# Kernel optimization log

Measured on AMD Instinct MI355X. Metric: run time of the kernel, lower is better.

Reference implementation:

```python
import jax, jax.numpy as jnp
import numpy as np

N = 50000      # nodes
E = 800000     # edges (avg degree 16)
F_IN = 3       # dataset.num_node_features
H = 256        # hidden_channels
G = 64         # batch_size (num graphs)
OUT = 24       # lin_out output dim


def setup_inputs() -> dict:
    key = jax.random.key(0)
    ks = jax.random.split(key, 16)
    s = 0.05
    inp = {
        "x": jax.random.normal(ks[0], (N, F_IN), jnp.float32),
        "edge_index": jax.random.randint(ks[1], (2, E), 0, N, dtype=jnp.int32),
        "batch": jnp.sort(jax.random.randint(ks[2], (N,), 0, G, dtype=jnp.int32)),
        # layer 1 (F_IN -> H)
        "w_rel1": jax.random.normal(ks[3], (F_IN, H), jnp.float32) * s,
        "w_root1": jax.random.normal(ks[4], (F_IN, H), jnp.float32) * s,
        "b1": jnp.zeros((H,), jnp.float32),
        # layers 2..7 (H -> H), stacked
        "w_rel": jax.random.normal(ks[5], (6, H, H), jnp.float32) * s,
        "w_root": jax.random.normal(ks[6], (6, H, H), jnp.float32) * s,
        "b": jnp.zeros((6, H), jnp.float32),
        # output head
        "w_out": jax.random.normal(ks[7], (H, OUT), jnp.float32) * s,
        "b_out": jnp.zeros((OUT,), jnp.float32),
    }
    return inp


def reference(x, edge_index, batch, w_rel1, w_root1, b1, w_rel, w_root, b, w_out, b_out):
    src, dst = edge_index[0], edge_index[1]

    def conv(h, wr, wro, bb):
        # PyG GraphConv with add aggregation:
        # out_i = W_rel @ sum_{j -> i} h_j + b + W_root @ h_i
        agg = jax.ops.segment_sum(h[src], dst, num_segments=N)
        return agg @ wr + h @ wro + bb

    h = jax.nn.relu(conv(x, w_rel1, w_root1, b1))
    for i in range(6):
        h = jax.nn.relu(conv(h, w_rel[i], w_root[i], b[i]))

    # global_mean_pool over batch segment ids
    counts = jax.ops.segment_sum(jnp.ones((N,), h.dtype), batch, num_segments=G)
    pooled = jax.ops.segment_sum(h, batch, num_segments=G) / jnp.maximum(counts, 1.0)[:, None]

    # dropout is identity in eval mode
    return pooled @ w_out + b_out
```

## Files before the change

kernel.cpp:

```cpp
#include <hip/hip_runtime.h>

#define N_NODES 50000
#define MPAD 50048
#define N_EDGES 800000
#define H 256
#define K_CAT 512
#define G_BATCH 64
#define OUT_DIM 24

#define SCAN_BLK 256
#define NBLK ((N_NODES + SCAN_BLK - 1) / SCAN_BLK)

typedef __attribute__((ext_vector_type(8))) short short8;
typedef __attribute__((ext_vector_type(4))) float float4v;

__device__ __forceinline__ float bf2f(unsigned short u) {
    return __uint_as_float(((unsigned)u) << 16);
}
__device__ __forceinline__ unsigned short f2bf(float f) {
    unsigned x = __float_as_uint(f);
    unsigned r = (x + 0x7FFFu + ((x >> 16) & 1u)) >> 16;
    return (unsigned short)r;
}

__device__ __forceinline__ void async_copy16(void* lds, const void* g) {
    __builtin_amdgcn_global_load_lds(
        (const __attribute__((address_space(1))) unsigned int*)g,
        (__attribute__((address_space(3))) unsigned int*)lds, 16, 0, 0);
}



__global__ void histo_kernel(const int* __restrict__ dst, int* __restrict__ deg,
                             int* __restrict__ epos) {
    int e = blockIdx.x * blockDim.x + threadIdx.x;
    if (e < N_EDGES) epos[e] = atomicAdd(&deg[dst[e]], 1);
}

__global__ void scan_block(const int* __restrict__ deg, int* __restrict__ rowptr,
                           int* __restrict__ blockSums) {
    __shared__ int s[SCAN_BLK];
    int idx = blockIdx.x * SCAN_BLK + threadIdx.x;
    int v = (idx < N_NODES) ? deg[idx] : 0;
    s[threadIdx.x] = v;
    __syncthreads();
    for (int off = 1; off < SCAN_BLK; off <<= 1) {
        int t = (threadIdx.x >= off) ? s[threadIdx.x - off] : 0;
        __syncthreads();
        s[threadIdx.x] += t;
        __syncthreads();
    }
    if (idx < N_NODES) rowptr[idx] = s[threadIdx.x] - v;
    if (threadIdx.x == SCAN_BLK - 1) blockSums[blockIdx.x] = s[threadIdx.x];
}

__global__ void scan_finish(int* __restrict__ rowptr, const int* __restrict__ blockSums) {
    __shared__ int s[SCAN_BLK];
    int t = threadIdx.x;
    int v = (t < NBLK) ? blockSums[t] : 0;
    s[t] = v;
    __syncthreads();
    for (int off = 1; off < SCAN_BLK; off <<= 1) {
        int tv = (t >= off) ? s[t - off] : 0;
        __syncthreads();
        s[t] += tv;
        __syncthreads();
    }
    int prefix = (blockIdx.x > 0) ? s[blockIdx.x - 1] : 0;
    int idx = blockIdx.x * SCAN_BLK + t;
    if (idx < N_NODES) rowptr[idx] += prefix;
    if (blockIdx.x == 0 && t == 0) rowptr[N_NODES] = s[NBLK - 1];
}

__global__ void fill_csr(const int* __restrict__ src, const int* __restrict__ dst,
                         const int* __restrict__ rowptr, const int* __restrict__ epos,
                         int* __restrict__ csr_src) {
    int e = blockIdx.x * blockDim.x + threadIdx.x;
    if (e >= N_EDGES) return;
    csr_src[rowptr[dst[e]] + epos[e]] = src[e];
}


__global__ void prep_weights(const float* __restrict__ w_rel, const float* __restrict__ w_root,
                             unsigned short* __restrict__ WcatT) {
    int idx = blockIdx.x * blockDim.x + threadIdx.x;
    if (idx >= 6 * K_CAT * H) return;
    int n = idx & (H - 1);
    int k = (idx >> 8) & (K_CAT - 1);
    int l = idx >> 17;
    float v;
    if (k < H) {
        int f = (k & 0xC0) | ((k & 3) << 4) | ((k >> 2) & 15);
        v = w_rel[(size_t)l * H * H + f * H + n];
    } else {
        v = w_root[(size_t)l * H * H + (k - H) * H + n];
    }
    WcatT[(size_t)l * H * K_CAT + (size_t)n * K_CAT + k] = f2bf(v);
}


__global__ void agg3(const float* __restrict__ x, const int* __restrict__ rowptr,
                     const int* __restrict__ csr_src, float* __restrict__ agg) {
    int n = blockIdx.x * blockDim.x + threadIdx.x;
    if (n >= N_NODES) return;
    int beg = rowptr[n], end = rowptr[n + 1];
    float a0 = 0.f, a1 = 0.f, a2 = 0.f;
    for (int i = beg; i < end; ++i) {
        int s = csr_src[i];
        a0 += x[s * 3 + 0];
        a1 += x[s * 3 + 1];
        a2 += x[s * 3 + 2];
    }
    agg[n * 3 + 0] = a0;
    agg[n * 3 + 1] = a1;
    agg[n * 3 + 2] = a2;
}

__global__ void layer1_kernel(const float* __restrict__ x, const float* __restrict__ agg,
                              const float* __restrict__ wr, const float* __restrict__ wro,
                              const float* __restrict__ bias, unsigned short* __restrict__ cat,
                              unsigned char* __restrict__ h8, float* __restrict__ hscale) {
    __shared__ unsigned char tmp[H];
    int n = blockIdx.x;
    int f = threadIdx.x;
    float a0 = agg[n * 3 + 0], a1 = agg[n * 3 + 1], a2 = agg[n * 3 + 2];
    float x0 = x[n * 3 + 0], x1 = x[n * 3 + 1], x2 = x[n * 3 + 2];
    float v = bias[f];
    v += a0 * wr[0 * H + f] + a1 * wr[1 * H + f] + a2 * wr[2 * H + f];
    v += x0 * wro[0 * H + f] + x1 * wro[1 * H + f] + x2 * wro[2 * H + f];
    v = fmaxf(v, 0.f);
    cat[(size_t)n * K_CAT + H + f] = f2bf(v);
    float m = v;
#pragma unroll
    for (int off = 1; off < 64; off <<= 1) m = fmaxf(m, __shfl_xor(m, off, 64));
    float inv = m > 0.f ? 255.f / m : 0.f;
    tmp[(f & 0xC0) | ((f & 15) << 2) | ((f >> 4) & 3)] = (unsigned char)(v * inv + 0.5f);
    if ((f & 63) == 0) hscale[n * 4 + (f >> 6)] = m * (1.f / 255.f);
    __syncthreads();
    if (f < 64) *(unsigned*)(h8 + (size_t)n * H + f * 4) = *(const unsigned*)(tmp + f * 4);
}


__global__ __launch_bounds__(256) void aggH(unsigned short* __restrict__ cat,
                                            const unsigned char* __restrict__ h8,
                                            const float* __restrict__ hscale,
                                            const int* __restrict__ rowptr,
                                            const int* __restrict__ csr_src) {
    int gtid = blockIdx.x * blockDim.x + threadIdx.x;
    int node = gtid >> 6;
    if (node >= N_NODES) return;
    int lane = threadIdx.x & 63;
    int sub = lane >> 4;
    int fl = lane & 15;
    int g = fl >> 2;
    int beg = rowptr[node], end = rowptr[node + 1];

    if (beg >= end) {
        if (sub == 0) {
            uint4 z = make_uint4(0, 0, 0, 0);
            unsigned short* o = cat + (size_t)node * K_CAT + fl * 16;
            *(uint4*)o = z;
            *(uint4*)(o + 8) = z;
        }
        return;
    }

    float acc[16] = {};
    const unsigned char* base = h8 + fl * 16;
    int last = end - 1;

    int i0 = beg + sub;
    int i1 = beg + 4 + sub;
    int i2 = beg + 8 + sub;
    int i3 = beg + 12 + sub;
    int s0 = csr_src[i0 < end ? i0 : last];
    int s1 = csr_src[i1 < end ? i1 : last];
    int s2 = csr_src[i2 < end ? i2 : last];
    int s3 = csr_src[i3 < end ? i3 : last];
    float sc0 = (i0 < end) ? hscale[s0 * 4 + g] : 0.f;
    float sc1 = (i1 < end) ? hscale[s1 * 4 + g] : 0.f;
    uint4 q0 = *(const uint4*)(base + (size_t)s0 * H);
    uint4 q1 = *(const uint4*)(base + (size_t)s1 * H);

    for (int i = beg; i < end; i += 4) {
        int i4 = i + 16 + sub;
        int s4 = csr_src[i4 < end ? i4 : last];
        int ic = i + 8 + sub;
        float sc2 = (ic < end) ? hscale[s2 * 4 + g] : 0.f;
        uint4 q2 = *(const uint4*)(base + (size_t)s2 * H);

        float sc = sc0;
        acc[0]  = fmaf((float)(q0.x & 0xffu), sc, acc[0]);
        acc[1]  = fmaf((float)((q0.x >> 8) & 0xffu), sc, acc[1]);
        acc[2]  = fmaf((float)((q0.x >> 16) & 0xffu), sc, acc[2]);
        acc[3]  = fmaf((float)(q0.x >> 24), sc, acc[3]);
        acc[4]  = fmaf((float)(q0.y & 0xffu), sc, acc[4]);
        acc[5]  = fmaf((float)((q0.y >> 8) & 0xffu), sc, acc[5]);
        acc[6]  = fmaf((float)((q0.y >> 16) & 0xffu), sc, acc[6]);
        acc[7]  = fmaf((float)(q0.y >> 24), sc, acc[7]);
        acc[8]  = fmaf((float)(q0.z & 0xffu), sc, acc[8]);
        acc[9]  = fmaf((float)((q0.z >> 8) & 0xffu), sc, acc[9]);
        acc[10] = fmaf((float)((q0.z >> 16) & 0xffu), sc, acc[10]);
        acc[11] = fmaf((float)(q0.z >> 24), sc, acc[11]);
        acc[12] = fmaf((float)(q0.w & 0xffu), sc, acc[12]);
        acc[13] = fmaf((float)((q0.w >> 8) & 0xffu), sc, acc[13]);
        acc[14] = fmaf((float)((q0.w >> 16) & 0xffu), sc, acc[14]);
        acc[15] = fmaf((float)(q0.w >> 24), sc, acc[15]);

        q0 = q1; q1 = q2;
        sc0 = sc1; sc1 = sc2;
        s2 = s3; s3 = s4;
    }

#pragma unroll
    for (int j = 0; j < 16; j++) {
        acc[j] += __shfl_xor(acc[j], 16, 64);
        acc[j] += __shfl_xor(acc[j], 32, 64);
    }

    if (sub == 0) {
        unsigned short* o = cat + (size_t)node * K_CAT + fl * 16;
        uint4 p0, p1;
        p0.x = (unsigned)f2bf(acc[0])  | ((unsigned)f2bf(acc[1]) << 16);
        p0.y = (unsigned)f2bf(acc[2])  | ((unsigned)f2bf(acc[3]) << 16);
        p0.z = (unsigned)f2bf(acc[4])  | ((unsigned)f2bf(acc[5]) << 16);
        p0.w = (unsigned)f2bf(acc[6])  | ((unsigned)f2bf(acc[7]) << 16);
        p1.x = (unsigned)f2bf(acc[8])  | ((unsigned)f2bf(acc[9]) << 16);
        p1.y = (unsigned)f2bf(acc[10]) | ((unsigned)f2bf(acc[11]) << 16);
        p1.z = (unsigned)f2bf(acc[12]) | ((unsigned)f2bf(acc[13]) << 16);
        p1.w = (unsigned)f2bf(acc[14]) | ((unsigned)f2bf(acc[15]) << 16);
        *(uint4*)o = p0;
        *(uint4*)(o + 8) = p1;
    }
}


#define GBM 64
#define GBN 128
#define GBK 64

__global__ __launch_bounds__(256) void gemm_mfma(
    const unsigned short* __restrict__ cat, const unsigned short* __restrict__ WcatT,
    const float* __restrict__ bias, unsigned short* __restrict__ catOut,
    unsigned char* __restrict__ h8, float* __restrict__ hscale) {
    __shared__ unsigned short sA[GBM][GBK];
    __shared__ unsigned short sB[GBN][GBK];

    const int tid = threadIdx.x;
    const int wave = tid >> 6;
    const int lane = tid & 63;
    const int quad = lane >> 4;
    const int l16 = lane & 15;
    const int wm0 = (wave & 1) * 32;
    const int wn0 = (wave >> 1) * 64;
    const int m0 = blockIdx.x * GBM;
    const int n0 = blockIdx.y * GBN;

    const int rowoff = lane >> 3;
    const int schunk = ((lane & 7) ^ rowoff) * 8;
    const unsigned short* Asrc[2];
    const unsigned short* Bsrc[4];
#pragma unroll
    for (int j = 0; j < 2; j++) {
        int q = wave * 2 + j;
        Asrc[j] = cat + (size_t)(m0 + q * 8 + rowoff) * K_CAT + schunk;
    }
#pragma unroll
    for (int j = 0; j < 4; j++) {
        int q = wave * 4 + j;
        Bsrc[j] = WcatT + (size_t)(n0 + q * 8 + rowoff) * K_CAT + schunk;
    }

    const int sw = l16 & 7;
    const int ca0 = (quad ^ sw) * 8;
    const int ca1 = ((4 + quad) ^ sw) * 8;

    float4v acc[2][4] = {};

    for (int kk = 0; kk < K_CAT; kk += GBK) {
#pragma unroll
        for (int j = 0; j < 2; j++)
            async_copy16((char*)sA + (wave * 2 + j) * 1024, Asrc[j] + kk);
#pragma unroll
        for (int j = 0; j < 4; j++)
            async_copy16((char*)sB + (wave * 4 + j) * 1024, Bsrc[j] + kk);
        __syncthreads();

        short8 a[2][2], b[4][2];
#pragma unroll
        for (int i = 0; i < 2; i++) {
            const unsigned short* ra = &sA[wm0 + i * 16 + l16][0];
            a[i][0] = *(const short8*)(ra + ca0);
            a[i][1] = *(const short8*)(ra + ca1);
        }
#pragma unroll
        for (int i = 0; i < 4; i++) {
            const unsigned short* rb = &sB[wn0 + i * 16 + l16][0];
            b[i][0] = *(const short8*)(rb + ca0);
            b[i][1] = *(const short8*)(rb + ca1);
        }
#pragma unroll
        for (int sub = 0; sub < 2; sub++)
#pragma unroll
            for (int mi = 0; mi < 2; mi++)
#pragma unroll
                for (int ni = 0; ni < 4; ni++)
                    acc[mi][ni] = __builtin_amdgcn_mfma_f32_16x16x32_bf16(
                        a[mi][sub], b[ni][sub], acc[mi][ni], 0, 0, 0);
        __syncthreads();
    }

    const int hb = n0 + wn0 + l16 * 4;
    const int gsc = (n0 + wn0) >> 6;
    float bcol[4];
#pragma unroll
    for (int ni = 0; ni < 4; ni++) bcol[ni] = bias[n0 + wn0 + ni * 16 + l16];

#pragma unroll
    for (int mi = 0; mi < 2; mi++) {
        int rowb = m0 + wm0 + mi * 16 + quad * 4;
#pragma unroll
        for (int r = 0; r < 4; r++) {
            int row = rowb + r;
            float v0 = fmaxf(acc[mi][0][r] + bcol[0], 0.f);
            float v1 = fmaxf(acc[mi][1][r] + bcol[1], 0.f);
            float v2 = fmaxf(acc[mi][2][r] + bcol[2], 0.f);
            float v3 = fmaxf(acc[mi][3][r] + bcol[3], 0.f);
            unsigned short* co = catOut + (size_t)row * K_CAT + H + n0 + wn0 + l16;
            co[0]  = f2bf(v0);
            co[16] = f2bf(v1);
            co[32] = f2bf(v2);
            co[48] = f2bf(v3);
            float m = fmaxf(fmaxf(v0, v1), fmaxf(v2, v3));
            m = fmaxf(m, __shfl_xor(m, 1, 64));
            m = fmaxf(m, __shfl_xor(m, 2, 64));
            m = fmaxf(m, __shfl_xor(m, 4, 64));
            m = fmaxf(m, __shfl_xor(m, 8, 64));
            float inv = m > 0.f ? 255.f / m : 0.f;
            unsigned p = (unsigned)(v0 * inv + 0.5f)
                       | ((unsigned)(v1 * inv + 0.5f) << 8)
                       | ((unsigned)(v2 * inv + 0.5f) << 16)
                       | ((unsigned)(v3 * inv + 0.5f) << 24);
            *(unsigned*)(h8 + (size_t)row * H + hb) = p;
            if (l16 == 0) hscale[row * 4 + gsc] = m * (1.f / 255.f);
        }
    }
}


__device__ __forceinline__ int lowerBound(const int* __restrict__ batch, int val) {
    int lo = 0, hi = N_NODES;
    while (lo < hi) {
        int mid = (lo + hi) >> 1;
        if (batch[mid] < val) lo = mid + 1; else hi = mid;
    }
    return lo;
}

__global__ void pool_partial(const unsigned short* __restrict__ cat, const int* __restrict__ batch,
                             float* __restrict__ pooled) {
    int g = blockIdx.x;
    int seg = blockIdx.y;
    int f = threadIdx.x;
    int start = lowerBound(batch, g);
    int end = lowerBound(batch, g + 1);
    int len = end - start;
    int s0 = start + (int)((long long)len * seg / 8);
    int s1 = start + (int)((long long)len * (seg + 1) / 8);
    float sum = 0.f;
    for (int n = s0; n < s1; ++n)
        sum += bf2f(cat[(size_t)n * K_CAT + H + f]);
    if (s1 > s0)
        atomicAdd(&pooled[g * H + f], sum);
}

__global__ void head_kernel(const float* __restrict__ pooled, const int* __restrict__ batch,
                            const float* __restrict__ w_out, const float* __restrict__ b_out,
                            float* __restrict__ out) {
    int g = blockIdx.x;
    int o = threadIdx.x;
    int start = lowerBound(batch, g);
    int end = lowerBound(batch, g + 1);
    float cnt = fmaxf((float)(end - start), 1.f);
    float sum = 0.f;
    for (int f = 0; f < H; ++f)
        sum += pooled[g * H + f] * w_out[f * OUT_DIM + o];
    out[g * OUT_DIM + o] = b_out[o] + sum / cnt;
}


extern "C" void kernel_launch(void* const* d_in, const int* in_sizes, int n_in,
                              void* d_out, int out_size, void* d_ws, size_t ws_size,
                              hipStream_t stream) {
    const float* x      = (const float*)d_in[0];
    const int*   ei     = (const int*)d_in[1];
    const int*   batch  = (const int*)d_in[2];
    const float* w_rel1 = (const float*)d_in[3];
    const float* w_root1= (const float*)d_in[4];
    const float* b1     = (const float*)d_in[5];
    const float* w_rel  = (const float*)d_in[6];
    const float* w_root = (const float*)d_in[7];
    const float* b      = (const float*)d_in[8];
    const float* w_out  = (const float*)d_in[9];
    const float* b_out  = (const float*)d_in[10];
    float* out = (float*)d_out;

    const int* src = ei;
    const int* dst = ei + N_EDGES;

    unsigned short* catA  = (unsigned short*)d_ws;
    unsigned short* catB  = catA + (size_t)MPAD * K_CAT;
    unsigned short* WcatT = catB + (size_t)MPAD * K_CAT;
    float* agg3buf = (float*)(WcatT + (size_t)6 * H * K_CAT);
    float* pooled  = agg3buf + (size_t)N_NODES * 4;
    float* hscale  = pooled + G_BATCH * H;
    int* rowptr    = (int*)(hscale + (size_t)MPAD * 4);
    int* degcur    = rowptr + (N_NODES + 1);
    int* blockSums = degcur + N_NODES;
    int* csr_src   = blockSums + SCAN_BLK;
    int* epos      = csr_src + N_EDGES;
    unsigned char* h8 = (unsigned char*)(epos + N_EDGES);

    hipMemsetAsync(degcur, 0, N_NODES * sizeof(int), stream);
    histo_kernel<<<(N_EDGES + 255) / 256, 256, 0, stream>>>(dst, degcur, epos);
    scan_block<<<NBLK, SCAN_BLK, 0, stream>>>(degcur, rowptr, blockSums);
    scan_finish<<<NBLK, SCAN_BLK, 0, stream>>>(rowptr, blockSums);
    fill_csr<<<(N_EDGES + 255) / 256, 256, 0, stream>>>(src, dst, rowptr, epos, csr_src);

    prep_weights<<<(6 * K_CAT * H + 255) / 256, 256, 0, stream>>>(w_rel, w_root, WcatT);

    agg3<<<(N_NODES + 255) / 256, 256, 0, stream>>>(x, rowptr, csr_src, agg3buf);
    layer1_kernel<<<N_NODES, H, 0, stream>>>(x, agg3buf, w_rel1, w_root1, b1, catA, h8, hscale);

    unsigned short* cur = catA;
    unsigned short* nxt = catB;
    for (int l = 0; l < 6; ++l) {
        aggH<<<(N_NODES * 64 + 255) / 256, 256, 0, stream>>>(cur, h8, hscale, rowptr, csr_src);
        dim3 grid(MPAD / GBM, H / GBN);
        gemm_mfma<<<grid, 256, 0, stream>>>(cur, WcatT + (size_t)l * H * K_CAT,
                                            b + (size_t)l * H, nxt, h8, hscale);
        unsigned short* t = cur; cur = nxt; nxt = t;
    }

    hipMemsetAsync(pooled, 0, G_BATCH * H * sizeof(float), stream);
    pool_partial<<<dim3(G_BATCH, 8), 256, 0, stream>>>(cur, batch, pooled);
    head_kernel<<<G_BATCH, OUT_DIM, 0, stream>>>(pooled, batch, w_out, b_out, out);
}
```

Baseline: 655.9 us.

## Drop bf16 root activations; dequantize int8 h in GEMM for root half

The bf16 copy of node features is no longer kept in the concatenated buffer. The GEMM now reads the aggregate half as bf16 and, for the root half, loads the int8 quantized features plus per-group scales, dequantizes them to bf16 in LDS, and uses permuted root weights to match the byte layout. Pooling and the head are adapted to the int8 layout. This cuts activation writes and reads per layer, but it adds dequantization ALU work inside the GEMM and adds quantization error to the root term.

```diff
diff --git a/kernel.cpp b/kernel.cpp
--- a/kernel.cpp
+++ b/kernel.cpp
@@ -93,7 +93,9 @@
         int f = (k & 0xC0) | ((k & 3) << 4) | ((k >> 2) & 15);
         v = w_rel[(size_t)l * H * H + f * H + n];
     } else {
-        v = w_root[(size_t)l * H * H + (k - H) * H + n];
+        int b = k - H;
+        int f = (b & 0xC0) | ((b & 3) << 4) | ((b >> 2) & 15);
+        v = w_root[(size_t)l * H * H + f * H + n];
     }
     WcatT[(size_t)l * H * K_CAT + (size_t)n * K_CAT + k] = f2bf(v);
 }
@@ -118,7 +120,7 @@
 
 __global__ void layer1_kernel(const float* __restrict__ x, const float* __restrict__ agg,
                               const float* __restrict__ wr, const float* __restrict__ wro,
-                              const float* __restrict__ bias, unsigned short* __restrict__ cat,
+                              const float* __restrict__ bias,
                               unsigned char* __restrict__ h8, float* __restrict__ hscale) {
     __shared__ unsigned char tmp[H];
     int n = blockIdx.x;
@@ -129,7 +131,6 @@
     v += a0 * wr[0 * H + f] + a1 * wr[1 * H + f] + a2 * wr[2 * H + f];
     v += x0 * wro[0 * H + f] + x1 * wro[1 * H + f] + x2 * wro[2 * H + f];
     v = fmaxf(v, 0.f);
-    cat[(size_t)n * K_CAT + H + f] = f2bf(v);
     float m = v;
 #pragma unroll
     for (int off = 1; off < 64; off <<= 1) m = fmaxf(m, __shfl_xor(m, off, 64));
@@ -141,7 +142,7 @@
 }
 
 
-__global__ __launch_bounds__(256) void aggH(unsigned short* __restrict__ cat,
+__global__ __launch_bounds__(256) void aggH(unsigned short* __restrict__ aggcat,
                                             const unsigned char* __restrict__ h8,
                                             const float* __restrict__ hscale,
                                             const int* __restrict__ rowptr,
@@ -158,7 +159,7 @@
     if (beg >= end) {
         if (sub == 0) {
             uint4 z = make_uint4(0, 0, 0, 0);
-            unsigned short* o = cat + (size_t)node * K_CAT + fl * 16;
+            unsigned short* o = aggcat + (size_t)node * H + fl * 16;
             *(uint4*)o = z;
             *(uint4*)(o + 8) = z;
         }
@@ -219,7 +220,7 @@
     }
 
     if (sub == 0) {
-        unsigned short* o = cat + (size_t)node * K_CAT + fl * 16;
+        unsigned short* o = aggcat + (size_t)node * H + fl * 16;
         uint4 p0, p1;
         p0.x = (unsigned)f2bf(acc[0])  | ((unsigned)f2bf(acc[1]) << 16);
         p0.y = (unsigned)f2bf(acc[2])  | ((unsigned)f2bf(acc[3]) << 16);
@@ -240,9 +241,10 @@
 #define GBK 64
 
 __global__ __launch_bounds__(256) void gemm_mfma(
-    const unsigned short* __restrict__ cat, const unsigned short* __restrict__ WcatT,
-    const float* __restrict__ bias, unsigned short* __restrict__ catOut,
-    unsigned char* __restrict__ h8, float* __restrict__ hscale) {
+    const unsigned short* __restrict__ aggcat, const unsigned char* __restrict__ h8in,
+    const float* __restrict__ hscin, const unsigned short* __restrict__ WcatT,
+    const float* __restrict__ bias,
+    unsigned char* __restrict__ h8out, float* __restrict__ hscout) {
     __shared__ unsigned short sA[GBM][GBK];
     __shared__ unsigned short sB[GBN][GBK];
 
@@ -258,12 +260,12 @@
 
     const int rowoff = lane >> 3;
     const int schunk = ((lane & 7) ^ rowoff) * 8;
-    const unsigned short* Asrc[2];
+    const unsigned short* Aagg[2];
     const unsigned short* Bsrc[4];
 #pragma unroll
     for (int j = 0; j < 2; j++) {
         int q = wave * 2 + j;
-        Asrc[j] = cat + (size_t)(m0 + q * 8 + rowoff) * K_CAT + schunk;
+        Aagg[j] = aggcat + (size_t)(m0 + q * 8 + rowoff) * H + schunk;
     }
 #pragma unroll
     for (int j = 0; j < 4; j++) {
@@ -271,44 +273,90 @@
         Bsrc[j] = WcatT + (size_t)(n0 + q * 8 + rowoff) * K_CAT + schunk;
     }
 
+    const int r_row = wave * 16 + (lane >> 3);
+    const int r_bc = lane & 7;
+    const unsigned char* r_src0 = h8in + (size_t)(m0 + r_row) * H + r_bc * 8;
+    const unsigned char* r_src1 = r_src0 + 8 * H;
+    const float* sc0p = hscin + (size_t)(m0 + r_row) * 4;
+    const float* sc1p = sc0p + 32;
+    const int ldsoff = wave * 2048 + (lane >> 3) * 128 + ((lane & 7) ^ (lane >> 3)) * 16;
+    unsigned short* ldst0 = (unsigned short*)((char*)sA + ldsoff);
+    unsigned short* ldst1 = (unsigned short*)((char*)sA + ldsoff + 1024);
+
     const int sw = l16 & 7;
     const int ca0 = (quad ^ sw) * 8;
     const int ca1 = ((4 + quad) ^ sw) * 8;
 
     float4v acc[2][4] = {};
 
-    for (int kk = 0; kk < K_CAT; kk += GBK) {
+#define COMPUTE()                                                            \
+    {                                                                        \
+        short8 a[2][2], b[4][2];                                             \
+        _Pragma("unroll") for (int i = 0; i < 2; i++) {                      \
+            const unsigned short* ra = &sA[wm0 + i * 16 + l16][0];           \
+            a[i][0] = *(const short8*)(ra + ca0);                            \
+            a[i][1] = *(const short8*)(ra + ca1);                            \
+        }                                                                    \
+        _Pragma("unroll") for (int i = 0; i < 4; i++) {                      \
+            const unsigned short* rb = &sB[wn0 + i * 16 + l16][0];           \
+            b[i][0] = *(const short8*)(rb + ca0);                            \
+            b[i][1] = *(const short8*)(rb + ca1);                            \
+        }                                                                    \
+        _Pragma("unroll") for (int sub = 0; sub < 2; sub++)                  \
+            _Pragma("unroll") for (int mi = 0; mi < 2; mi++)                 \
+                _Pragma("unroll") for (int ni = 0; ni < 4; ni++)             \
+                    acc[mi][ni] = __builtin_amdgcn_mfma_f32_16x16x32_bf16(   \
+                        a[mi][sub], b[ni][sub], acc[mi][ni], 0, 0, 0);       \
+    }
+
+    for (int kk = 0; kk < 256; kk += GBK) {
 #pragma unroll
         for (int j = 0; j < 2; j++)
-            async_copy16((char*)sA + (wave * 2 + j) * 1024, Asrc[j] + kk);
+            async_copy16((char*)sA + (wave * 2 + j) * 1024, Aagg[j] + kk);
 #pragma unroll
         for (int j = 0; j < 4; j++)
             async_copy16((char*)sB + (wave * 4 + j) * 1024, Bsrc[j] + kk);
         __syncthreads();
-
-        short8 a[2][2], b[4][2];
-#pragma unroll
-        for (int i = 0; i < 2; i++) {
-            const unsigned short* ra = &sA[wm0 + i * 16 + l16][0];
-            a[i][0] = *(const short8*)(ra + ca0);
-            a[i][1] = *(const short8*)(ra + ca1);
+        COMPUTE();
+        __syncthreads();
+    }
+
+#pragma unroll
+    for (int kb = 0; kb < 4; kb++) {
+        const int kk = 256 + kb * GBK;
+#pragma unroll
+        for (int j = 0; j < 4; j++)
+            async_copy16((char*)sB + (wave * 4 + j) * 1024, Bsrc[j] + kk);
+        {
+            uint2 q0 = *(const uint2*)(r_src0 + kb * GBK);
+            uint2 q1 = *(const uint2*)(r_src1 + kb * GBK);
+            float s0 = sc0p[kb];
+            float s1 = sc1p[kb];
+            uint4 p0, p1;
+            p0.x = (unsigned)f2bf((float)(q0.x & 0xffu) * s0)
+                 | ((unsigned)f2bf((float)((q0.x >> 8) & 0xffu) * s0) << 16);
+            p0.y = (unsigned)f2bf((float)((q0.x >> 16) & 0xffu) * s0)
+                 | ((unsigned)f2bf((float)(q0.x >> 24) * s0) << 16);
+            p0.z = (unsigned)f2bf((float)(q0.y & 0xffu) * s0)
+                 | ((unsigned)f2bf((float)((q0.y >> 8) & 0xffu) * s0) << 16);
+            p0.w = (unsigned)f2bf((float)((q0.y >> 16) & 0xffu) * s0)
+                 | ((unsigned)f2bf((float)(q0.y >> 24) * s0) << 16);
+            p1.x = (unsigned)f2bf((float)(q1.x & 0xffu) * s1)
+                 | ((unsigned)f2bf((float)((q1.x >> 8) & 0xffu) * s1) << 16);
+            p1.y = (unsigned)f2bf((float)((q1.x >> 16) & 0xffu) * s1)
+                 | ((unsigned)f2bf((float)(q1.x >> 24) * s1) << 16);
+            p1.z = (unsigned)f2bf((float)(q1.y & 0xffu) * s1)
+                 | ((unsigned)f2bf((float)((q1.y >> 8) & 0xffu) * s1) << 16);
+            p1.w = (unsigned)f2bf((float)((q1.y >> 16) & 0xffu) * s1)
+                 | ((unsigned)f2bf((float)(q1.y >> 24) * s1) << 16);
+            *(uint4*)ldst0 = p0;
+            *(uint4*)ldst1 = p1;
         }
-#pragma unroll
-        for (int i = 0; i < 4; i++) {
-            const unsigned short* rb = &sB[wn0 + i * 16 + l16][0];
-            b[i][0] = *(const short8*)(rb + ca0);
-            b[i][1] = *(const short8*)(rb + ca1);
-        }
-#pragma unroll
-        for (int sub = 0; sub < 2; sub++)
-#pragma unroll
-            for (int mi = 0; mi < 2; mi++)
-#pragma unroll
-                for (int ni = 0; ni < 4; ni++)
-                    acc[mi][ni] = __builtin_amdgcn_mfma_f32_16x16x32_bf16(
-                        a[mi][sub], b[ni][sub], acc[mi][ni], 0, 0, 0);
-        __syncthreads();
-    }
+        __syncthreads();
+        COMPUTE();
+        __syncthreads();
+    }
+#undef COMPUTE
 
     const int hb = n0 + wn0 + l16 * 4;
     const int gsc = (n0 + wn0) >> 6;
@@ -326,11 +374,6 @@
             float v1 = fmaxf(acc[mi][1][r] + bcol[1], 0.f);
             float v2 = fmaxf(acc[mi][2][r] + bcol[2], 0.f);
             float v3 = fmaxf(acc[mi][3][r] + bcol[3], 0.f);
-            unsigned short* co = catOut + (size_t)row * K_CAT + H + n0 + wn0 + l16;
-            co[0]  = f2bf(v0);
-            co[16] = f2bf(v1);
-            co[32] = f2bf(v2);
-            co[48] = f2bf(v3);
             float m = fmaxf(fmaxf(v0, v1), fmaxf(v2, v3));
             m = fmaxf(m, __shfl_xor(m, 1, 64));
             m = fmaxf(m, __shfl_xor(m, 2, 64));
@@ -341,8 +384,8 @@
                        | ((unsigned)(v1 * inv + 0.5f) << 8)
                        | ((unsigned)(v2 * inv + 0.5f) << 16)
                        | ((unsigned)(v3 * inv + 0.5f) << 24);
-            *(unsigned*)(h8 + (size_t)row * H + hb) = p;
-            if (l16 == 0) hscale[row * 4 + gsc] = m * (1.f / 255.f);
+            *(unsigned*)(h8out + (size_t)row * H + hb) = p;
+            if (l16 == 0) hscout[row * 4 + gsc] = m * (1.f / 255.f);
         }
     }
 }
@@ -357,11 +400,13 @@
     return lo;
 }
 
-__global__ void pool_partial(const unsigned short* __restrict__ cat, const int* __restrict__ batch,
-                             float* __restrict__ pooled) {
+__global__ void pool_partial(const unsigned char* __restrict__ h8,
+                             const float* __restrict__ hscale,
+                             const int* __restrict__ batch, float* __restrict__ pooled) {
     int g = blockIdx.x;
     int seg = blockIdx.y;
-    int f = threadIdx.x;
+    int bpos = threadIdx.x;
+    int grp = bpos >> 6;
     int start = lowerBound(batch, g);
     int end = lowerBound(batch, g + 1);
     int len = end - start;
@@ -369,9 +414,9 @@
     int s1 = start + (int)((long long)len * (seg + 1) / 8);
     float sum = 0.f;
     for (int n = s0; n < s1; ++n)
-        sum += bf2f(cat[(size_t)n * K_CAT + H + f]);
+        sum += (float)h8[(size_t)n * H + bpos] * hscale[n * 4 + grp];
     if (s1 > s0)
-        atomicAdd(&pooled[g * H + f], sum);
+        atomicAdd(&pooled[g * H + bpos], sum);
 }
 
 __global__ void head_kernel(const float* __restrict__ pooled, const int* __restrict__ batch,
@@ -383,8 +428,10 @@
     int end = lowerBound(batch, g + 1);
     float cnt = fmaxf((float)(end - start), 1.f);
     float sum = 0.f;
-    for (int f = 0; f < H; ++f)
-        sum += pooled[g * H + f] * w_out[f * OUT_DIM + o];
+    for (int bpos = 0; bpos < H; ++bpos) {
+        int f = (bpos & 0xC0) | ((bpos & 3) << 4) | ((bpos >> 2) & 15);
+        sum += pooled[g * H + bpos] * w_out[f * OUT_DIM + o];
+    }
     out[g * OUT_DIM + o] = b_out[o] + sum / cnt;
 }
 
@@ -408,18 +455,19 @@
     const int* src = ei;
     const int* dst = ei + N_EDGES;
 
-    unsigned short* catA  = (unsigned short*)d_ws;
-    unsigned short* catB  = catA + (size_t)MPAD * K_CAT;
-    unsigned short* WcatT = catB + (size_t)MPAD * K_CAT;
-    float* agg3buf = (float*)(WcatT + (size_t)6 * H * K_CAT);
+    unsigned short* aggcat = (unsigned short*)d_ws;
+    unsigned short* WcatT  = aggcat + (size_t)MPAD * H;
+    unsigned char* h8a = (unsigned char*)(WcatT + (size_t)6 * H * K_CAT);
+    unsigned char* h8b = h8a + (size_t)MPAD * H;
+    float* hsa     = (float*)(h8b + (size_t)MPAD * H);
+    float* hsb     = hsa + (size_t)MPAD * 4;
+    float* agg3buf = hsb + (size_t)MPAD * 4;
     float* pooled  = agg3buf + (size_t)N_NODES * 4;
-    float* hscale  = pooled + G_BATCH * H;
-    int* rowptr    = (int*)(hscale + (size_t)MPAD * 4);
+    int* rowptr    = (int*)(pooled + G_BATCH * H);
     int* degcur    = rowptr + (N_NODES + 1);
     int* blockSums = degcur + N_NODES;
     int* csr_src   = blockSums + SCAN_BLK;
     int* epos      = csr_src + N_EDGES;
-    unsigned char* h8 = (unsigned char*)(epos + N_EDGES);
 
     hipMemsetAsync(degcur, 0, N_NODES * sizeof(int), stream);
     histo_kernel<<<(N_EDGES + 255) / 256, 256, 0, stream>>>(dst, degcur, epos);
@@ -430,19 +478,21 @@
     prep_weights<<<(6 * K_CAT * H + 255) / 256, 256, 0, stream>>>(w_rel, w_root, WcatT);
 
     agg3<<<(N_NODES + 255) / 256, 256, 0, stream>>>(x, rowptr, csr_src, agg3buf);
-    layer1_kernel<<<N_NODES, H, 0, stream>>>(x, agg3buf, w_rel1, w_root1, b1, catA, h8, hscale);
-
-    unsigned short* cur = catA;
-    unsigned short* nxt = catB;
+    layer1_kernel<<<N_NODES, H, 0, stream>>>(x, agg3buf, w_rel1, w_root1, b1, h8a, hsa);
+
+    unsigned char* h8c = h8a; float* hsc = hsa;
+    unsigned char* h8n = h8b; float* hsn = hsb;
     for (int l = 0; l < 6; ++l) {
-        aggH<<<(N_NODES * 64 + 255) / 256, 256, 0, stream>>>(cur, h8, hscale, rowptr, csr_src);
+        aggH<<<(N_NODES * 64 + 255) / 256, 256, 0, stream>>>(aggcat, h8c, hsc, rowptr, csr_src);
         dim3 grid(MPAD / GBM, H / GBN);
-        gemm_mfma<<<grid, 256, 0, stream>>>(cur, WcatT + (size_t)l * H * K_CAT,
-                                            b + (size_t)l * H, nxt, h8, hscale);
-        unsigned short* t = cur; cur = nxt; nxt = t;
+        gemm_mfma<<<grid, 256, 0, stream>>>(aggcat, h8c, hsc,
+                                            WcatT + (size_t)l * H * K_CAT,
+                                            b + (size_t)l * H, h8n, hsn);
+        unsigned char* t8 = h8c; h8c = h8n; h8n = t8;
+        float* tf = hsc; hsc = hsn; hsn = tf;
     }
 
     hipMemsetAsync(pooled, 0, G_BATCH * H * sizeof(float), stream);
-    pool_partial<<<dim3(G_BATCH, 8), 256, 0, stream>>>(cur, batch, pooled);
+    pool_partial<<<dim3(G_BATCH, 8), 256, 0, stream>>>(h8c, hsc, batch, pooled);
     head_kernel<<<G_BATCH, OUT_DIM, 0, stream>>>(pooled, batch, w_out, b_out, out);
 }
```

Result: faster. 626.8 us (-4.4%).
